# Kernel tuning notes

Hardware: AMD Instinct MI355X
Metric: run time of the kernel (lower is better)

Reference implementation:

```python
import jax, jax.numpy as jnp
import numpy as np

B, L, D = 16, 1024, 256  # batch, c_len == q_len (required by the expand/add in the source), 2*d_model


def mask_logits(x, m):
    # Faithful to the source's (unusual) masking: x*m + x*(1-m)*1e30
    return x * m + x * (1.0 - m) * 1e30


def setup_inputs() -> dict:
    key = jax.random.key(0)
    k = jax.random.split(key, 7)
    c = jax.random.normal(k[0], (B, L, D), dtype=jnp.float32)
    q = jax.random.normal(k[1], (B, L, D), dtype=jnp.float32)
    c_mask = jnp.ones((B, 1, L), dtype=jnp.float32)
    q_mask = jnp.ones((B, 1, L), dtype=jnp.float32)
    # Learned parameters (nn.Parameter zeros in the source; random here so the test is non-degenerate)
    c_weight = jax.random.normal(k[2], (D, 1), dtype=jnp.float32) * 0.05
    q_weight = jax.random.normal(k[3], (D, 1), dtype=jnp.float32) * 0.05
    cq_weight = jax.random.normal(k[4], (1, 1, D), dtype=jnp.float32) * 0.05
    bias = jnp.zeros((1,), dtype=jnp.float32)
    return {"c": c, "q": q, "c_mask": c_mask, "q_mask": q_mask,
            "c_weight": c_weight, "q_weight": q_weight,
            "cq_weight": cq_weight, "bias": bias}


def reference(c, q, c_mask, q_mask, c_weight, q_weight, cq_weight, bias):
    # Dropout treated as identity (inference) for a deterministic reference.
    s0 = jnp.matmul(c, c_weight)                      # [B, L, 1] -> broadcasts over q_len
    s1 = jnp.swapaxes(jnp.matmul(c, q_weight), 1, 2)  # [B, 1, L] (source uses c here, not q)
    s2 = jnp.einsum('bid,bjd->bij', c * cq_weight, q) # [B, L, L]
    S = s0 + s1 + s2 + bias                           # trilinear similarity
    S1 = jax.nn.softmax(mask_logits(S, q_mask), axis=-1)              # [B, Lc, Lq]
    C2Q = jnp.matmul(S1, q)                                           # [B, Lc, D]
    # torch F.softmax with no dim on a 3D tensor defaults to dim=0 (legacy behavior) -> axis=0
    S2 = jax.nn.softmax(mask_logits(jnp.swapaxes(S, 1, 2), c_mask), axis=0)  # [B, Lq, Lc]
    S2 = jnp.matmul(S1, S2)                                           # [B, Lc, Lc]
    Q2C = jnp.matmul(S2, c)                                           # [B, Lc, D]
    # torch.cat default dim=0 -> [4B, Lc, D]
    return jnp.concatenate((c, C2Q, c * C2Q, c * Q2C), axis=0)
```

## Files before the change

kernel.cpp:

```cpp
#include <hip/hip_runtime.h>

typedef __bf16 bf16;
typedef _Float16 f16;
typedef __attribute__((ext_vector_type(8))) __bf16 bf16x8;
typedef __attribute__((ext_vector_type(4))) __bf16 bf16x4;
typedef __attribute__((ext_vector_type(8))) _Float16 f16x8;
typedef __attribute__((ext_vector_type(4))) _Float16 f16x4;
typedef __attribute__((ext_vector_type(4))) float f32x4;

constexpr int Bn = 16, Ln = 1024, Dn = 256;

__device__ __forceinline__ float maskf(float m) { return m + (1.0f - m) * 1e30f; }

__device__ __forceinline__ void gload16(const void* g, void* l) {
  __builtin_amdgcn_global_load_lds((const __attribute__((address_space(1))) void*)g,
                                   (__attribute__((address_space(3))) void*)l, 16, 0, 0);
}

#define VMCNT(N) asm volatile("s_waitcnt vmcnt(" #N ")" ::: "memory")
#define LGKM0 asm volatile("s_waitcnt lgkmcnt(0)" ::: "memory")
#define BARR                                  \
  do {                                        \
    asm volatile("" ::: "memory");            \
    __builtin_amdgcn_s_barrier();             \
    asm volatile("" ::: "memory");            \
  } while (0)

__device__ __forceinline__ void stageB128(const bf16* __restrict__ B, int ldb, int k0,
                                          bf16* lB, int tid, int wid) {
#pragma unroll
  for (int p = 0; p < 2; ++p) {
    int c0 = tid + (p << 8);
    int row = c0 >> 2, kk = (c0 & 3) << 3;
    gload16(B + (size_t)row * ldb + k0 + kk, lB + ((p << 8) + (wid << 6)) * 8);
  }
}

__global__ __launch_bounds__(256) void k_prep2(
    const float* __restrict__ c, const float* __restrict__ q,
    const float* __restrict__ cw, const float* __restrict__ qw,
    const float* __restrict__ cqw, bf16* __restrict__ cm, bf16* __restrict__ qb,
    bf16* __restrict__ cT, bf16* __restrict__ qT,
    float* __restrict__ s0, float* __restrict__ s1, float* __restrict__ outc) {
  __shared__ __align__(16) bf16 tc[32][264];
  __shared__ __align__(16) bf16 tq[32][264];
  int blk = blockIdx.x;
  int b = blk >> 5;
  int l0 = (blk & 31) << 5;
  int t = threadIdx.x;
  int rl = t >> 3;
  int c0 = (t & 7) << 5;
  int grow = b * Ln + l0 + rl;
  size_t base = (size_t)grow * Dn + c0;
  float4 cv[8], qv[8];
#pragma unroll
  for (int k = 0; k < 8; ++k) {
    cv[k] = *(const float4*)&c[base + k * 4];
    qv[k] = *(const float4*)&q[base + k * 4];
  }
  float d0 = 0.f, d1 = 0.f;
#pragma unroll
  for (int k = 0; k < 8; ++k) {
    float4 w = *(const float4*)&cw[c0 + k * 4];
    float4 u = *(const float4*)&qw[c0 + k * 4];
    d0 += cv[k].x * w.x + cv[k].y * w.y + cv[k].z * w.z + cv[k].w * w.w;
    d1 += cv[k].x * u.x + cv[k].y * u.y + cv[k].z * u.z + cv[k].w * u.w;
  }
  d0 += __shfl_xor(d0, 1); d0 += __shfl_xor(d0, 2); d0 += __shfl_xor(d0, 4);
  d1 += __shfl_xor(d1, 1); d1 += __shfl_xor(d1, 2); d1 += __shfl_xor(d1, 4);
  if ((t & 7) == 0) { s0[grow] = d0; s1[grow] = d1; }
#pragma unroll
  for (int k = 0; k < 8; ++k) *(float4*)&outc[base + k * 4] = cv[k];
#pragma unroll
  for (int k2 = 0; k2 < 4; ++k2) {
    float4 m0 = *(const float4*)&cqw[c0 + k2 * 8];
    float4 m1 = *(const float4*)&cqw[c0 + k2 * 8 + 4];
    bf16x8 vm, vq, vc;
#pragma unroll
    for (int e = 0; e < 8; ++e) {
      float cvv = ((const float*)&cv[k2 * 2 + (e >> 2)])[e & 3];
      float qvv = ((const float*)&qv[k2 * 2 + (e >> 2)])[e & 3];
      float mw = (e < 4) ? ((const float*)&m0)[e] : ((const float*)&m1)[e - 4];
      vm[e] = (bf16)(cvv * mw);
      vq[e] = (bf16)qvv;
      vc[e] = (bf16)cvv;
    }
    *(bf16x8*)&cm[base + k2 * 8] = vm;
    *(bf16x8*)&qb[base + k2 * 8] = vq;
    *(bf16x8*)&tc[rl][c0 + k2 * 8] = vc;
    *(bf16x8*)&tq[rl][c0 + k2 * 8] = vq;
  }
  __syncthreads();
  int d = t;
  size_t tb = ((size_t)b * Dn + d) * Ln + l0;
  bf16x8 o[4];
#pragma unroll
  for (int j = 0; j < 4; ++j)
#pragma unroll
    for (int e = 0; e < 8; ++e) o[j][e] = tc[j * 8 + e][d];
#pragma unroll
  for (int j = 0; j < 4; ++j) *(bf16x8*)&cT[tb + j * 8] = o[j];
#pragma unroll
  for (int j = 0; j < 4; ++j)
#pragma unroll
    for (int e = 0; e < 8; ++e) o[j][e] = tq[j * 8 + e][d];
#pragma unroll
  for (int j = 0; j < 4; ++j) *(bf16x8*)&qT[tb + j * 8] = o[j];
}

__global__ __launch_bounds__(256) void g_s(const bf16* __restrict__ Am,
                                           const bf16* __restrict__ Bm,
                                           const float* __restrict__ s0,
                                           const float* __restrict__ s1,
                                           const float* __restrict__ bias,
                                           f16* __restrict__ S) {
  __shared__ __align__(16) bf16 lds[2][256 * 32];
  int f = blockIdx.x;
  int o = (f & 7) * 128 + (f >> 3);
  int bx = o & 7, by = (o >> 3) & 7, b = o >> 6;
  const bf16* Ab = Am + (size_t)b * Ln * Dn + (size_t)by * 128 * Dn;
  const bf16* Bb = Bm + (size_t)b * Ln * Dn + (size_t)bx * 128 * Dn;
  const int tid = threadIdx.x, wid = tid >> 6, lane = tid & 63;
  const int r = lane & 15, h = lane >> 4, wr = wid >> 1, wc = wid & 1;
  f32x4 acc[4][4];
  f32x4 zero = {0.f, 0.f, 0.f, 0.f};
#pragma unroll
  for (int i = 0; i < 4; ++i)
#pragma unroll
    for (int j = 0; j < 4; ++j) acc[i][j] = zero;

  stageB128(Ab, Dn, 0, &lds[0][0], tid, wid);
  stageB128(Bb, Dn, 0, &lds[0][128 * 32], tid, wid);
  for (int t = 0; t < 8; ++t) {
    int cur = t & 1;
    if (t < 7) {
      stageB128(Ab, Dn, (t + 1) * 32, &lds[cur ^ 1][0], tid, wid);
      stageB128(Bb, Dn, (t + 1) * 32, &lds[cur ^ 1][128 * 32], tid, wid);
      VMCNT(4);
    } else {
      VMCNT(0);
    }
    BARR;
    const bf16* lA = &lds[cur][0];
    const bf16* lB = &lds[cur][128 * 32];
    bf16x8 av[4], bv[4];
#pragma unroll
    for (int i = 0; i < 4; ++i) {
      av[i] = *(const bf16x8*)(lA + ((wr << 6) + (i << 4) + r) * 32 + (h << 3));
      bv[i] = *(const bf16x8*)(lB + ((wc << 6) + (i << 4) + r) * 32 + (h << 3));
    }
#pragma unroll
    for (int i = 0; i < 4; ++i)
#pragma unroll
      for (int j = 0; j < 4; ++j)
        acc[i][j] = __builtin_amdgcn_mfma_f32_16x16x32_bf16(av[i], bv[j], acc[i][j], 0, 0, 0);
    LGKM0; BARR;
  }
  int grow = by * 128 + wr * 64, gcol = bx * 128 + wc * 64;
  float bvv = bias[0];
  size_t sb = (size_t)b * Ln * Ln;
#pragma unroll
  for (int j = 0; j < 4; ++j) {
    int n = gcol + j * 16 + r;
    float v1 = s1[b * Ln + n];
#pragma unroll
    for (int i = 0; i < 4; ++i) {
      int mb = grow + i * 16 + h * 4;
#pragma unroll
      for (int g = 0; g < 4; ++g) {
        float v0 = s0[b * Ln + mb + g];
        S[sb + (size_t)(mb + g) * Ln + n] = (f16)(acc[i][j][g] + v0 + v1 + bvv);
      }
    }
  }
}

__global__ __launch_bounds__(256) void k_rowsoftmax(const f16* __restrict__ S,
                                                    const float* __restrict__ qmask,
                                                    bf16* __restrict__ P1) {
  int t = threadIdx.x;
  int row = blockIdx.x * 4 + (t >> 6);
  int b = row >> 10;
  int lane = t & 63;
  const f16* Sr = S + (size_t)row * Ln;
  const float* qm = qmask + (size_t)b * Ln;
  float v[16];
  float mx = -3.4e38f;
#pragma unroll
  for (int p = 0; p < 2; ++p) {
    f16x8 x = ((const f16x8*)Sr)[lane + (p << 6)];
    float4 m0 = ((const float4*)qm)[(lane + (p << 6)) * 2];
    float4 m1 = ((const float4*)qm)[(lane + (p << 6)) * 2 + 1];
    float mm[8] = {m0.x, m0.y, m0.z, m0.w, m1.x, m1.y, m1.z, m1.w};
#pragma unroll
    for (int e = 0; e < 8; ++e) {
      float xv = (float)x[e] * maskf(mm[e]);
      v[8 * p + e] = xv;
      mx = fmaxf(mx, xv);
    }
  }
#pragma unroll
  for (int off = 32; off; off >>= 1) mx = fmaxf(mx, __shfl_xor(mx, off));
  float sum = 0.f;
#pragma unroll
  for (int k = 0; k < 16; ++k) {
    v[k] = __expf(v[k] - mx);
    sum += v[k];
  }
#pragma unroll
  for (int off = 32; off; off >>= 1) sum += __shfl_xor(sum, off);
  float inv = 1.0f / sum;
  bf16* Pr = P1 + (size_t)row * Ln;
#pragma unroll
  for (int p = 0; p < 2; ++p) {
    bf16x8 o;
#pragma unroll
    for (int e = 0; e < 8; ++e) o[e] = (bf16)(v[8 * p + e] * inv);
    ((bf16x8*)Pr)[lane + (p << 6)] = o;
  }
}

__global__ __launch_bounds__(256) void k_bp2(const f16* __restrict__ S,
                                             const float* __restrict__ cmask,
                                             bf16* __restrict__ P2) {
  __shared__ __align__(16) bf16 tile[16][32][36];
  int i0 = blockIdx.y * 32, j0 = blockIdx.x * 32;
  int t = threadIdx.x;
  int ti = t >> 3, tj4 = (t & 7) << 2;
  int i = i0 + ti;
  const f16* Sp = S + (size_t)i * Ln + j0 + tj4;
  float fm[16];
#pragma unroll
  for (int b = 0; b < 16; ++b) fm[b] = maskf(cmask[b * Ln + i]);
  f16x4 u[16];
#pragma unroll
  for (int b = 0; b < 16; ++b) u[b] = *(const f16x4*)(Sp + (size_t)b * Ln * Ln);
  float m[4] = {-3.4e38f, -3.4e38f, -3.4e38f, -3.4e38f};
#pragma unroll
  for (int b = 0; b < 16; ++b)
#pragma unroll
    for (int g = 0; g < 4; ++g) m[g] = fmaxf(m[g], (float)u[b][g] * fm[b]);
  float e[16][4];
  float s[4] = {0.f, 0.f, 0.f, 0.f};
#pragma unroll
  for (int b = 0; b < 16; ++b)
#pragma unroll
    for (int g = 0; g < 4; ++g) {
      e[b][g] = __expf((float)u[b][g] * fm[b] - m[g]);
      s[g] += e[b][g];
    }
#pragma unroll
  for (int g = 0; g < 4; ++g) s[g] = 1.0f / s[g];
#pragma unroll
  for (int b = 0; b < 16; ++b)
#pragma unroll
    for (int g = 0; g < 4; ++g) tile[b][tj4 + g][ti] = (bf16)(e[b][g] * s[g]);
  __syncthreads();
  int jl = t >> 3, i4 = (t & 7) << 2;
#pragma unroll
  for (int b = 0; b < 16; ++b) {
    *(bf16x4*)&P2[((size_t)b * Ln + j0 + jl) * Ln + i0 + i4] =
        *(const bf16x4*)&tile[b][jl][i4];
  }
}

__global__ __launch_bounds__(256) void g_t(const bf16* __restrict__ cT,
                                           const bf16* __restrict__ P2,
                                           bf16* __restrict__ TT) {
  __shared__ __align__(16) bf16 lds[2][256 * 32];
  int f = blockIdx.x;
  int o = (f & 7) * 32 + (f >> 3);
  int b = o >> 4, md = (o >> 3) & 1, nb = o & 7;
  const bf16* Ab = cT + (size_t)b * Dn * Ln + (size_t)md * 128 * Ln;
  const bf16* Bb = P2 + (size_t)b * Ln * Ln + (size_t)nb * 128 * Ln;
  const int tid = threadIdx.x, wid = tid >> 6, lane = tid & 63;
  const int r = lane & 15, h = lane >> 4, wr = wid >> 1, wc = wid & 1;
  f32x4 acc[4][4];
  f32x4 zero = {0.f, 0.f, 0.f, 0.f};
#pragma unroll
  for (int i = 0; i < 4; ++i)
#pragma unroll
    for (int j = 0; j < 4; ++j) acc[i][j] = zero;

  stageB128(Ab, Ln, 0, &lds[0][0], tid, wid);
  stageB128(Bb, Ln, 0, &lds[0][128 * 32], tid, wid);
  for (int t = 0; t < 32; ++t) {
    int cur = t & 1;
    if (t < 31) {
      stageB128(Ab, Ln, (t + 1) * 32, &lds[cur ^ 1][0], tid, wid);
      stageB128(Bb, Ln, (t + 1) * 32, &lds[cur ^ 1][128 * 32], tid, wid);
      VMCNT(4);
    } else {
      VMCNT(0);
    }
    BARR;
    const bf16* lA = &lds[cur][0];
    const bf16* lB = &lds[cur][128 * 32];
    bf16x8 av[4], bv[4];
#pragma unroll
    for (int i = 0; i < 4; ++i) {
      av[i] = *(const bf16x8*)(lA + ((wr << 6) + (i << 4) + r) * 32 + (h << 3));
      bv[i] = *(const bf16x8*)(lB + ((wc << 6) + (i << 4) + r) * 32 + (h << 3));
    }
#pragma unroll
    for (int i = 0; i < 4; ++i)
#pragma unroll
      for (int j = 0; j < 4; ++j)
        acc[i][j] = __builtin_amdgcn_mfma_f32_16x16x32_bf16(av[i], bv[j], acc[i][j], 0, 0, 0);
    LGKM0; BARR;
  }
  size_t ob = (size_t)b * Dn * Ln;
  int dbase = md * 128 + wr * 64, cbase = nb * 128 + wc * 64;
#pragma unroll
  for (int i = 0; i < 4; ++i)
#pragma unroll
    for (int j = 0; j < 4; ++j) {
      int n = cbase + j * 16 + r;
#pragma unroll
      for (int g = 0; g < 4; ++g)
        TT[ob + (size_t)(dbase + i * 16 + h * 4 + g) * Ln + n] = (bf16)acc[i][j][g];
    }
}

__global__ __launch_bounds__(256) void g_cq(const bf16* __restrict__ P1,
                                            const bf16* __restrict__ qT,
                                            const bf16* __restrict__ TT,
                                            const float* __restrict__ c,
                                            float* __restrict__ out) {
  __shared__ __align__(16) bf16 lds[2][384 * 32];
  int f = blockIdx.x;
  int o = (f & 7) * 32 + (f >> 3);
  int b = o >> 4, by = (o >> 1) & 7, bx = o & 1;
  const bf16* Ab = P1 + (size_t)b * Ln * Ln + (size_t)by * 128 * Ln;
  const bf16* B1 = qT + (size_t)b * Dn * Ln + (size_t)bx * 128 * Ln;
  const bf16* B2 = TT + (size_t)b * Dn * Ln + (size_t)bx * 128 * Ln;
  const int tid = threadIdx.x, wid = tid >> 6, lane = tid & 63;
  const int r = lane & 15, h = lane >> 4, wr = wid >> 1, wc = wid & 1;
  f32x4 acc1[4][4], acc2[4][4];
  f32x4 zero = {0.f, 0.f, 0.f, 0.f};
#pragma unroll
  for (int i = 0; i < 4; ++i)
#pragma unroll
    for (int j = 0; j < 4; ++j) { acc1[i][j] = zero; acc2[i][j] = zero; }

  stageB128(Ab, Ln, 0, &lds[0][0], tid, wid);
  stageB128(B1, Ln, 0, &lds[0][4096], tid, wid);
  stageB128(B2, Ln, 0, &lds[0][8192], tid, wid);
  for (int t = 0; t < 32; ++t) {
    int cur = t & 1;
    if (t < 31) {
      stageB128(Ab, Ln, (t + 1) * 32, &lds[cur ^ 1][0], tid, wid);
      stageB128(B1, Ln, (t + 1) * 32, &lds[cur ^ 1][4096], tid, wid);
      stageB128(B2, Ln, (t + 1) * 32, &lds[cur ^ 1][8192], tid, wid);
      VMCNT(6);
    } else {
      VMCNT(0);
    }
    BARR;
    const bf16* lA = &lds[cur][0];
    const bf16* lB1 = &lds[cur][4096];
    const bf16* lB2 = &lds[cur][8192];
    bf16x8 av[4], bv[4];
#pragma unroll
    for (int i = 0; i < 4; ++i)
      av[i] = *(const bf16x8*)(lA + ((wr << 6) + (i << 4) + r) * 32 + (h << 3));
#pragma unroll
    for (int j = 0; j < 4; ++j)
      bv[j] = *(const bf16x8*)(lB1 + ((wc << 6) + (j << 4) + r) * 32 + (h << 3));
#pragma unroll
    for (int i = 0; i < 4; ++i)
#pragma unroll
      for (int j = 0; j < 4; ++j)
        acc1[i][j] = __builtin_amdgcn_mfma_f32_16x16x32_bf16(av[i], bv[j], acc1[i][j], 0, 0, 0);
#pragma unroll
    for (int j = 0; j < 4; ++j)
      bv[j] = *(const bf16x8*)(lB2 + ((wc << 6) + (j << 4) + r) * 32 + (h << 3));
#pragma unroll
    for (int i = 0; i < 4; ++i)
#pragma unroll
      for (int j = 0; j < 4; ++j)
        acc2[i][j] = __builtin_amdgcn_mfma_f32_16x16x32_bf16(av[i], bv[j], acc2[i][j], 0, 0, 0);
    LGKM0; BARR;
  }

  int grow = by * 128 + wr * 64, gcol = bx * 128 + wc * 64;
  const float* cb = c + (size_t)b * Ln * Dn;
  float* o1 = out + (size_t)(1 * Bn + b) * Ln * Dn;
  float* o2 = out + (size_t)(2 * Bn + b) * Ln * Dn;
  float* o3 = out + (size_t)(3 * Bn + b) * Ln * Dn;
#pragma unroll
  for (int j = 0; j < 4; ++j) {
    int n = gcol + j * 16 + r;
#pragma unroll
    for (int i = 0; i < 4; ++i) {
      int mb = grow + i * 16 + h * 4;
#pragma unroll
      for (int g = 0; g < 4; ++g) {
        float v1 = acc1[i][j][g];
        float v2 = acc2[i][j][g];
        size_t off = (size_t)(mb + g) * Dn + n;
        float cc = cb[off];
        o1[off] = v1;
        o2[off] = cc * v1;
        o3[off] = cc * v2;
      }
    }
  }
}

extern "C" void kernel_launch(void* const* d_in, const int* in_sizes, int n_in,
                              void* d_out, int out_size, void* d_ws, size_t ws_size,
                              hipStream_t stream) {
  const float* c = (const float*)d_in[0];
  const float* q = (const float*)d_in[1];
  const float* cmask = (const float*)d_in[2];
  const float* qmask = (const float*)d_in[3];
  const float* cw = (const float*)d_in[4];
  const float* qw = (const float*)d_in[5];
  const float* cqw = (const float*)d_in[6];
  const float* bias = (const float*)d_in[7];
  float* out = (float*)d_out;

  char* w = (char*)d_ws;
  f16* S = (f16*)w;       w += (size_t)Bn * Ln * Ln * 2;
  bf16* P1 = (bf16*)w;    w += (size_t)Bn * Ln * Ln * 2;
  bf16* P2 = (bf16*)w;    w += (size_t)Bn * Ln * Ln * 2;
  bf16* cm = (bf16*)w;    w += (size_t)Bn * Ln * Dn * 2;
  bf16* qb = (bf16*)w;    w += (size_t)Bn * Ln * Dn * 2;
  bf16* cT = (bf16*)w;    w += (size_t)Bn * Dn * Ln * 2;
  bf16* qT = (bf16*)w;    w += (size_t)Bn * Dn * Ln * 2;
  bf16* TT = (bf16*)w;    w += (size_t)Bn * Dn * Ln * 2;
  float* s0 = (float*)w;  w += (size_t)Bn * Ln * 4;
  float* s1 = (float*)w;  w += (size_t)Bn * Ln * 4;
  if ((size_t)(w - (char*)d_ws) > ws_size) return;

  k_prep2<<<dim3(Bn * Ln / 32), 256, 0, stream>>>(c, q, cw, qw, cqw, cm, qb, cT, qT, s0, s1, out);
  g_s<<<dim3(1024), 256, 0, stream>>>(cm, qb, s0, s1, bias, S);
  k_rowsoftmax<<<dim3(Bn * Ln / 4), 256, 0, stream>>>(S, qmask, P1);
  k_bp2<<<dim3(Ln / 32, Ln / 32), 256, 0, stream>>>(S, cmask, P2);
  g_t<<<dim3(256), 256, 0, stream>>>(cT, P2, TT);
  g_cq<<<dim3(256), 256, 0, stream>>>(P1, qT, TT, c, out);
}
```

Measured before the change: 134.1 us.

## Use 512-thread blocks, K=64 tiles and XOR-swizzled LDS in g_t and g_cq

The two back-end GEMM kernels now use 8 waves per block instead of 4, each wave computing a 64x32 sub-tile. K-step tiles grow from 32 to 64, halving the number of loop iterations and barriers. LDS rows are XOR-swizzled by row to avoid bank conflicts on the wider rows. The aims are better latency hiding with more waves and fewer barriers, at the cost of doubled LDS use (96KB for g_cq) and less register reuse per wave.

```diff
diff --git a/kernel.cpp b/kernel.cpp
--- a/kernel.cpp
+++ b/kernel.cpp
@@ -34,6 +34,21 @@
     int row = c0 >> 2, kk = (c0 & 3) << 3;
     gload16(B + (size_t)row * ldb + k0 + kk, lB + ((p << 8) + (wid << 6)) * 8);
   }
+}
+
+__device__ __forceinline__ void stage512(const bf16* __restrict__ G, int ldg, int k0,
+                                         bf16* L, int tid, int wid) {
+#pragma unroll
+  for (int p = 0; p < 2; ++p) {
+    int u = tid + (p << 9);
+    int row = u >> 3, s = u & 7;
+    int kk = ((s ^ (row & 7)) << 3);
+    gload16(G + (size_t)row * ldg + k0 + kk, L + ((p << 9) + (wid << 6)) * 8);
+  }
+}
+
+__device__ __forceinline__ const bf16* swzp(const bf16* L, int row, int slot) {
+  return L + row * 64 + ((slot ^ (row & 7)) << 3);
 }
 
 __global__ __launch_bounds__(256) void k_prep2(
@@ -264,57 +279,62 @@
   }
 }
 
-__global__ __launch_bounds__(256) void g_t(const bf16* __restrict__ cT,
+__global__ __launch_bounds__(512) void g_t(const bf16* __restrict__ cT,
                                            const bf16* __restrict__ P2,
                                            bf16* __restrict__ TT) {
-  __shared__ __align__(16) bf16 lds[2][256 * 32];
+  __shared__ __align__(16) bf16 lds[2][2 * 128 * 64];
   int f = blockIdx.x;
   int o = (f & 7) * 32 + (f >> 3);
   int b = o >> 4, md = (o >> 3) & 1, nb = o & 7;
   const bf16* Ab = cT + (size_t)b * Dn * Ln + (size_t)md * 128 * Ln;
   const bf16* Bb = P2 + (size_t)b * Ln * Ln + (size_t)nb * 128 * Ln;
   const int tid = threadIdx.x, wid = tid >> 6, lane = tid & 63;
-  const int r = lane & 15, h = lane >> 4, wr = wid >> 1, wc = wid & 1;
-  f32x4 acc[4][4];
+  const int r = lane & 15, h = lane >> 4, wr = wid >> 2, wc = wid & 3;
+  f32x4 acc[4][2];
   f32x4 zero = {0.f, 0.f, 0.f, 0.f};
 #pragma unroll
   for (int i = 0; i < 4; ++i)
 #pragma unroll
-    for (int j = 0; j < 4; ++j) acc[i][j] = zero;
-
-  stageB128(Ab, Ln, 0, &lds[0][0], tid, wid);
-  stageB128(Bb, Ln, 0, &lds[0][128 * 32], tid, wid);
-  for (int t = 0; t < 32; ++t) {
+    for (int j = 0; j < 2; ++j) acc[i][j] = zero;
+
+  stage512(Ab, Ln, 0, &lds[0][0], tid, wid);
+  stage512(Bb, Ln, 0, &lds[0][8192], tid, wid);
+  for (int t = 0; t < 16; ++t) {
     int cur = t & 1;
-    if (t < 31) {
-      stageB128(Ab, Ln, (t + 1) * 32, &lds[cur ^ 1][0], tid, wid);
-      stageB128(Bb, Ln, (t + 1) * 32, &lds[cur ^ 1][128 * 32], tid, wid);
+    if (t < 15) {
+      stage512(Ab, Ln, (t + 1) * 64, &lds[cur ^ 1][0], tid, wid);
+      stage512(Bb, Ln, (t + 1) * 64, &lds[cur ^ 1][8192], tid, wid);
       VMCNT(4);
     } else {
       VMCNT(0);
     }
     BARR;
     const bf16* lA = &lds[cur][0];
-    const bf16* lB = &lds[cur][128 * 32];
-    bf16x8 av[4], bv[4];
-#pragma unroll
-    for (int i = 0; i < 4; ++i) {
-      av[i] = *(const bf16x8*)(lA + ((wr << 6) + (i << 4) + r) * 32 + (h << 3));
-      bv[i] = *(const bf16x8*)(lB + ((wc << 6) + (i << 4) + r) * 32 + (h << 3));
-    }
-#pragma unroll
-    for (int i = 0; i < 4; ++i)
-#pragma unroll
-      for (int j = 0; j < 4; ++j)
-        acc[i][j] = __builtin_amdgcn_mfma_f32_16x16x32_bf16(av[i], bv[j], acc[i][j], 0, 0, 0);
+    const bf16* lB = &lds[cur][8192];
+#pragma unroll
+    for (int kk2 = 0; kk2 < 2; ++kk2) {
+      int slot = (kk2 << 2) | h;
+      bf16x8 av[4], bv[2];
+#pragma unroll
+      for (int i = 0; i < 4; ++i)
+        av[i] = *(const bf16x8*)swzp(lA, (wr << 6) + (i << 4) + r, slot);
+#pragma unroll
+      for (int j = 0; j < 2; ++j)
+        bv[j] = *(const bf16x8*)swzp(lB, (wc << 5) + (j << 4) + r, slot);
+#pragma unroll
+      for (int i = 0; i < 4; ++i)
+#pragma unroll
+        for (int j = 0; j < 2; ++j)
+          acc[i][j] = __builtin_amdgcn_mfma_f32_16x16x32_bf16(av[i], bv[j], acc[i][j], 0, 0, 0);
+    }
     LGKM0; BARR;
   }
   size_t ob = (size_t)b * Dn * Ln;
-  int dbase = md * 128 + wr * 64, cbase = nb * 128 + wc * 64;
+  int dbase = md * 128 + wr * 64, cbase = nb * 128 + wc * 32;
 #pragma unroll
   for (int i = 0; i < 4; ++i)
 #pragma unroll
-    for (int j = 0; j < 4; ++j) {
+    for (int j = 0; j < 2; ++j) {
       int n = cbase + j * 16 + r;
 #pragma unroll
       for (int g = 0; g < 4; ++g)
@@ -322,12 +342,12 @@
     }
 }
 
-__global__ __launch_bounds__(256) void g_cq(const bf16* __restrict__ P1,
+__global__ __launch_bounds__(512) void g_cq(const bf16* __restrict__ P1,
                                             const bf16* __restrict__ qT,
                                             const bf16* __restrict__ TT,
                                             const float* __restrict__ c,
                                             float* __restrict__ out) {
-  __shared__ __align__(16) bf16 lds[2][384 * 32];
+  __shared__ __align__(16) bf16 lds[2][3 * 128 * 64];
   int f = blockIdx.x;
   int o = (f & 7) * 32 + (f >> 3);
   int b = o >> 4, by = (o >> 1) & 7, bx = o & 1;
@@ -335,61 +355,65 @@
   const bf16* B1 = qT + (size_t)b * Dn * Ln + (size_t)bx * 128 * Ln;
   const bf16* B2 = TT + (size_t)b * Dn * Ln + (size_t)bx * 128 * Ln;
   const int tid = threadIdx.x, wid = tid >> 6, lane = tid & 63;
-  const int r = lane & 15, h = lane >> 4, wr = wid >> 1, wc = wid & 1;
-  f32x4 acc1[4][4], acc2[4][4];
+  const int r = lane & 15, h = lane >> 4, wr = wid >> 2, wc = wid & 3;
+  f32x4 acc1[4][2], acc2[4][2];
   f32x4 zero = {0.f, 0.f, 0.f, 0.f};
 #pragma unroll
   for (int i = 0; i < 4; ++i)
 #pragma unroll
-    for (int j = 0; j < 4; ++j) { acc1[i][j] = zero; acc2[i][j] = zero; }
-
-  stageB128(Ab, Ln, 0, &lds[0][0], tid, wid);
-  stageB128(B1, Ln, 0, &lds[0][4096], tid, wid);
-  stageB128(B2, Ln, 0, &lds[0][8192], tid, wid);
-  for (int t = 0; t < 32; ++t) {
+    for (int j = 0; j < 2; ++j) { acc1[i][j] = zero; acc2[i][j] = zero; }
+
+  stage512(Ab, Ln, 0, &lds[0][0], tid, wid);
+  stage512(B1, Ln, 0, &lds[0][8192], tid, wid);
+  stage512(B2, Ln, 0, &lds[0][16384], tid, wid);
+  for (int t = 0; t < 16; ++t) {
     int cur = t & 1;
-    if (t < 31) {
-      stageB128(Ab, Ln, (t + 1) * 32, &lds[cur ^ 1][0], tid, wid);
-      stageB128(B1, Ln, (t + 1) * 32, &lds[cur ^ 1][4096], tid, wid);
-      stageB128(B2, Ln, (t + 1) * 32, &lds[cur ^ 1][8192], tid, wid);
+    if (t < 15) {
+      stage512(Ab, Ln, (t + 1) * 64, &lds[cur ^ 1][0], tid, wid);
+      stage512(B1, Ln, (t + 1) * 64, &lds[cur ^ 1][8192], tid, wid);
+      stage512(B2, Ln, (t + 1) * 64, &lds[cur ^ 1][16384], tid, wid);
       VMCNT(6);
     } else {
       VMCNT(0);
     }
     BARR;
     const bf16* lA = &lds[cur][0];
-    const bf16* lB1 = &lds[cur][4096];
-    const bf16* lB2 = &lds[cur][8192];
-    bf16x8 av[4], bv[4];
-#pragma unroll
-    for (int i = 0; i < 4; ++i)
-      av[i] = *(const bf16x8*)(lA + ((wr << 6) + (i << 4) + r) * 32 + (h << 3));
-#pragma unroll
-    for (int j = 0; j < 4; ++j)
-      bv[j] = *(const bf16x8*)(lB1 + ((wc << 6) + (j << 4) + r) * 32 + (h << 3));
-#pragma unroll
-    for (int i = 0; i < 4; ++i)
-#pragma unroll
-      for (int j = 0; j < 4; ++j)
-        acc1[i][j] = __builtin_amdgcn_mfma_f32_16x16x32_bf16(av[i], bv[j], acc1[i][j], 0, 0, 0);
-#pragma unroll
-    for (int j = 0; j < 4; ++j)
-      bv[j] = *(const bf16x8*)(lB2 + ((wc << 6) + (j << 4) + r) * 32 + (h << 3));
-#pragma unroll
-    for (int i = 0; i < 4; ++i)
-#pragma unroll
-      for (int j = 0; j < 4; ++j)
-        acc2[i][j] = __builtin_amdgcn_mfma_f32_16x16x32_bf16(av[i], bv[j], acc2[i][j], 0, 0, 0);
+    const bf16* lB1 = &lds[cur][8192];
+    const bf16* lB2 = &lds[cur][16384];
+#pragma unroll
+    for (int kk2 = 0; kk2 < 2; ++kk2) {
+      int slot = (kk2 << 2) | h;
+      bf16x8 av[4], bv[2];
+#pragma unroll
+      for (int i = 0; i < 4; ++i)
+        av[i] = *(const bf16x8*)swzp(lA, (wr << 6) + (i << 4) + r, slot);
+#pragma unroll
+      for (int j = 0; j < 2; ++j)
+        bv[j] = *(const bf16x8*)swzp(lB1, (wc << 5) + (j << 4) + r, slot);
+#pragma unroll
+      for (int i = 0; i < 4; ++i)
+#pragma unroll
+        for (int j = 0; j < 2; ++j)
+          acc1[i][j] = __builtin_amdgcn_mfma_f32_16x16x32_bf16(av[i], bv[j], acc1[i][j], 0, 0, 0);
+#pragma unroll
+      for (int j = 0; j < 2; ++j)
+        bv[j] = *(const bf16x8*)swzp(lB2, (wc << 5) + (j << 4) + r, slot);
+#pragma unroll
+      for (int i = 0; i < 4; ++i)
+#pragma unroll
+        for (int j = 0; j < 2; ++j)
+          acc2[i][j] = __builtin_amdgcn_mfma_f32_16x16x32_bf16(av[i], bv[j], acc2[i][j], 0, 0, 0);
+    }
     LGKM0; BARR;
   }
 
-  int grow = by * 128 + wr * 64, gcol = bx * 128 + wc * 64;
+  int grow = by * 128 + wr * 64, gcol = bx * 128 + wc * 32;
   const float* cb = c + (size_t)b * Ln * Dn;
   float* o1 = out + (size_t)(1 * Bn + b) * Ln * Dn;
   float* o2 = out + (size_t)(2 * Bn + b) * Ln * Dn;
   float* o3 = out + (size_t)(3 * Bn + b) * Ln * Dn;
 #pragma unroll
-  for (int j = 0; j < 4; ++j) {
+  for (int j = 0; j < 2; ++j) {
     int n = gcol + j * 16 + r;
 #pragma unroll
     for (int i = 0; i < 4; ++i) {
@@ -438,6 +462,6 @@
   g_s<<<dim3(1024), 256, 0, stream>>>(cm, qb, s0, s1, bias, S);
   k_rowsoftmax<<<dim3(Bn * Ln / 4), 256, 0, stream>>>(S, qmask, P1);
   k_bp2<<<dim3(Ln / 32, Ln / 32), 256, 0, stream>>>(S, cmask, P2);
-  g_t<<<dim3(256), 256, 0, stream>>>(cT, P2, TT);
-  g_cq<<<dim3(256), 256, 0, stream>>>(P1, qT, TT, c, out);
-}
+  g_t<<<dim3(256), 512, 0, stream>>>(cT, P2, TT);
+  g_cq<<<dim3(256), 512, 0, stream>>>(P1, qT, TT, c, out);
+}
```

New measurement: 117.6 us. 1.14x faster.
